# Optimization experiments

Measured on AMD Instinct MI355X. Metric: run time of the kernel, lower is better.

The kernel has to match this reference:

```python
import jax, jax.numpy as jnp
import numpy as np
from jax import lax

B, H, W, C, NH = 16, 56, 56, 192, 6
L = H * W
DH = C // NH            # 32
HID = 4 * C             # 768
ETA = 1.0 / DH          # TTT inner-loop learning rate
EPS = 1e-5

# ---- RoPE rotation tables (deterministic buffer, shape (H, W, C//2)) ----
_kmax = C // 4
_theta = 1.0 / (10000.0 ** (np.arange(_kmax) / _kmax))
_ii, _jj = np.meshgrid(np.arange(H), np.arange(W), indexing='ij')
_ang = np.concatenate([_ii[..., None] * _theta, _jj[..., None] * _theta], axis=-1)  # (H,W,C/2)
_COS = jnp.asarray(np.cos(_ang), dtype=jnp.float32)
_SIN = jnp.asarray(np.sin(_ang), dtype=jnp.float32)


def layernorm(x, g, b):
    mu = jnp.mean(x, axis=-1, keepdims=True)
    var = jnp.mean(jnp.square(x - mu), axis=-1, keepdims=True)
    return (x - mu) * lax.rsqrt(var + EPS) * g + b


def dwconv3x3(x_blc, w, b):
    # x: (B, L, Ch) -> depthwise 3x3 conv over (H, W) -> (B, L, Ch)
    Ch = x_blc.shape[-1]
    xi = x_blc.reshape(B, H, W, Ch).transpose(0, 3, 1, 2)  # NCHW
    y = lax.conv_general_dilated(xi, w, (1, 1), 'SAME', feature_group_count=Ch,
                                 dimension_numbers=('NCHW', 'OIHW', 'NCHW'))
    y = y + b[None, :, None, None]
    return y.transpose(0, 2, 3, 1).reshape(B, L, Ch)


def rope(x):
    # x: (B, L, C); rotate complex pairs with 2D axial angles
    xr = x.reshape(B, H, W, C // 2, 2)
    re, im = xr[..., 0], xr[..., 1]
    o_re = _COS * re - _SIN * im
    o_im = _SIN * re + _COS * im
    return jnp.stack([o_re, o_im], axis=-1).reshape(B, L, C)


def ttt_attn(xn, qkv_w, qkv_b, W0, proj_w, proj_b):
    qkv = xn @ qkv_w.T + qkv_b                      # (B, L, 3C)
    q, k, v = jnp.split(qkv, 3, axis=-1)
    q = rope(q) * (DH ** -0.5)
    k = rope(k)

    def to_heads(t):  # (B,L,C) -> (L, B*NH, DH)
        return t.reshape(B, L, NH, DH).transpose(1, 0, 2, 3).reshape(L, B * NH, DH)
    qs, ks, vs = to_heads(q), to_heads(k), to_heads(v)

    Wst0 = jnp.broadcast_to(W0[None], (B, NH, DH, DH)).reshape(B * NH, DH, DH)

    def step(Wst, qkv_t):
        qt, kt, vt = qkv_t
        pred = jnp.einsum('bij,bj->bi', Wst, kt)
        Wn = Wst - ETA * (pred - vt)[:, :, None] * kt[:, None, :]
        ot = jnp.einsum('bij,bj->bi', Wn, qt)
        return Wn, ot

    _, out = lax.scan(step, Wst0, (qs, ks, vs))     # out: (L, B*NH, DH)
    out = out.reshape(L, B, NH, DH).transpose(1, 0, 2, 3).reshape(B, L, C)
    return out @ proj_w.T + proj_b


def setup_inputs() -> dict:
    key = jax.random.key(0)
    ks = jax.random.split(key, 12)
    s = 0.02
    return {
        'x': jax.random.normal(ks[0], (B, L, C), jnp.float32),
        'cpe_w': jax.random.normal(ks[1], (C, 1, 3, 3), jnp.float32) * s,
        'cpe_b': jnp.zeros((C,), jnp.float32),
        'n1_g': jnp.ones((C,), jnp.float32),
        'n1_b': jnp.zeros((C,), jnp.float32),
        'qkv_w': jax.random.normal(ks[2], (3 * C, C), jnp.float32) * s,
        'qkv_b': jnp.zeros((3 * C,), jnp.float32),
        'W0': jax.random.normal(ks[3], (NH, DH, DH), jnp.float32) * s,
        'proj_w': jax.random.normal(ks[4], (C, C), jnp.float32) * s,
        'proj_b': jnp.zeros((C,), jnp.float32),
        'n2_g': jnp.ones((C,), jnp.float32),
        'n2_b': jnp.zeros((C,), jnp.float32),
        'fc1_w': jax.random.normal(ks[5], (HID, C), jnp.float32) * s,
        'fc1_b': jnp.zeros((HID,), jnp.float32),
        'dwc_w': jax.random.normal(ks[6], (HID, 1, 3, 3), jnp.float32) * s,
        'dwc_b': jnp.zeros((HID,), jnp.float32),
        'fc2_w': jax.random.normal(ks[7], (C, HID), jnp.float32) * s,
        'fc2_b': jnp.zeros((C,), jnp.float32),
    }


def reference(x, cpe_w, cpe_b, n1_g, n1_b, qkv_w, qkv_b, W0, proj_w, proj_b,
              n2_g, n2_b, fc1_w, fc1_b, dwc_w, dwc_b, fc2_w, fc2_b):
    # CPE: conditional positional encoding (depthwise conv residual)
    x = x + dwconv3x3(x, cpe_w, cpe_b)
    # TTT attention branch
    x = x + ttt_attn(layernorm(x, n1_g, n1_b), qkv_w, qkv_b, W0, proj_w, proj_b)
    # MLP branch with depthwise conv
    h1 = jax.nn.gelu(layernorm(x, n2_g, n2_b) @ fc1_w.T + fc1_b, approximate=False)
    h1 = jax.nn.gelu(h1 + dwconv3x3(h1, dwc_w, dwc_b), approximate=False)
    x = x + (h1 @ fc2_w.T + fc2_b)
    return x
```

## Files before the change

### kernel.cpp

```cpp
#include <hip/hip_runtime.h>
#include <hip/hip_bf16.h>

#define Bc 16
#define Hc 56
#define Wcc 56
#define Cc 192
#define NHc 6
#define Lc 3136
#define DHc 32
#define HIDc 768
#define NHEAD 96
#define Sc 32
#define NCHUNK 98
#define NPAIR (NHEAD*NCHUNK)
#define ROWS (Bc*Lc)
#define GR2 (ROWS/2)
#define ETAc (1.0f/32.0f)

typedef unsigned short u16;
typedef unsigned int u32;
typedef __attribute__((ext_vector_type(8))) short bf16x8;
typedef __attribute__((ext_vector_type(4))) float f32x4;
typedef __attribute__((ext_vector_type(16))) float f32x16;

__device__ __forceinline__ float b2f(u16 v){ u32 u = ((u32)v)<<16; float f; __builtin_memcpy(&f,&u,4); return f; }
__device__ __forceinline__ u16 f2b(float f){ u32 u; __builtin_memcpy(&u,&f,4); u32 r = u + 0x7FFFu + ((u>>16)&1u); return (u16)(r>>16); }
__device__ __forceinline__ f32x16 zero16(){ f32x16 z = {0,0,0,0,0,0,0,0,0,0,0,0,0,0,0,0}; return z; }

__device__ __forceinline__ void make_bfrags(const f32x16& t, int hi, bf16x8& b1, bf16x8& b2){
  u32 P[8], S[8];
  #pragma unroll
  for (int q=0;q<4;q++){
    #pragma unroll
    for (int j=0;j<2;j++){
      u32 r; float lo = t[4*q+2*j], hv = t[4*q+2*j+1];
      asm("v_cvt_pk_bf16_f32 %0, %1, %2" : "=v"(r) : "v"(lo), "v"(hv));
      P[2*q+j] = r;
    }
  }
  #pragma unroll
  for (int i=0;i<8;i++) S[i] = (u32)__shfl_xor((int)P[i], 32);
  union { u32 u[4]; bf16x8 v; } f1, f2;
  if (hi==0){ f1.u[0]=P[0]; f1.u[1]=P[1]; f1.u[2]=S[0]; f1.u[3]=S[1];
              f2.u[0]=P[4]; f2.u[1]=P[5]; f2.u[2]=S[4]; f2.u[3]=S[5]; }
  else      { f1.u[0]=S[2]; f1.u[1]=S[3]; f1.u[2]=P[2]; f1.u[3]=P[3];
              f2.u[0]=S[6]; f2.u[1]=S[7]; f2.u[2]=P[6]; f2.u[3]=P[7]; }
  b1 = f1.v; b2 = f2.v;
}

__global__ __launch_bounds__(256) void cast_bf16_kernel(const float* __restrict__ src, u16* __restrict__ dst, int n){
  int i = blockIdx.x*256 + threadIdx.x;
  if (i < n) dst[i] = f2b(src[i]);
}

__global__ __launch_bounds__(256) void dwt_kernel(const float* __restrict__ w, float* __restrict__ wt, int CH){
  int i = blockIdx.x*256 + threadIdx.x;
  if (i < CH*9){ int ch = i/9, t = i - ch*9; wt[t*CH + ch] = w[i]; }
}

__global__ __launch_bounds__(256) void rope_tab_kernel(float* __restrict__ ct, float* __restrict__ st){
  int i = blockIdx.x*256 + threadIdx.x;
  int l = i/96, p = i - l*96;
  int h = l/Wcc, w = l - h*Wcc;
  int kk = (p<48)? p : p-48;
  float th = powf(10000.f, -(float)kk/48.f);
  float ang = (float)((p<48)? h : w) * th;
  ct[i] = cosf(ang);
  st[i] = sinf(ang);
}

__global__ __launch_bounds__(256) void cpe_kernel(const float* __restrict__ x, const float* __restrict__ cwt9,
                                                  const float* __restrict__ bs, u16* __restrict__ x1){
  int gid = blockIdx.x*256 + threadIdx.x;
  int cg = gid % 24; int row = gid / 24; int ch0 = cg*8;
  int l = row % Lc; int h = l/Wcc, w = l - h*Wcc;
  const float* xp = x + (size_t)row*Cc + ch0;
  float acc[8];
  { f32x4 b0 = *(const f32x4*)(bs+ch0), b1v = *(const f32x4*)(bs+ch0+4);
    acc[0]=b0[0];acc[1]=b0[1];acc[2]=b0[2];acc[3]=b0[3];
    acc[4]=b1v[0];acc[5]=b1v[1];acc[6]=b1v[2];acc[7]=b1v[3]; }
  #pragma unroll
  for (int kh=0;kh<3;kh++){
    int hh = h+kh-1; if (hh<0 || hh>=Hc) continue;
    #pragma unroll
    for (int kw=0;kw<3;kw++){
      int ww = w+kw-1; if (ww<0 || ww>=Wcc) continue;
      const float* ip = xp + ((kh-1)*Wcc + (kw-1))*Cc;
      f32x4 i0 = *(const f32x4*)ip, i1 = *(const f32x4*)(ip+4);
      const float* wp = cwt9 + (kh*3+kw)*Cc + ch0;
      f32x4 w0 = *(const f32x4*)wp, w1 = *(const f32x4*)(wp+4);
      acc[0] += i0[0]*w0[0]; acc[1] += i0[1]*w0[1]; acc[2] += i0[2]*w0[2]; acc[3] += i0[3]*w0[3];
      acc[4] += i1[0]*w1[0]; acc[5] += i1[1]*w1[1]; acc[6] += i1[2]*w1[2]; acc[7] += i1[3]*w1[3];
    }
  }
  f32x4 c0 = *(const f32x4*)xp, c1 = *(const f32x4*)(xp+4);
  union { bf16x8 v; u16 s[8]; } ov;
  ov.s[0]=f2b(c0[0]+acc[0]); ov.s[1]=f2b(c0[1]+acc[1]); ov.s[2]=f2b(c0[2]+acc[2]); ov.s[3]=f2b(c0[3]+acc[3]);
  ov.s[4]=f2b(c1[0]+acc[4]); ov.s[5]=f2b(c1[1]+acc[5]); ov.s[6]=f2b(c1[2]+acc[6]); ov.s[7]=f2b(c1[3]+acc[7]);
  *(bf16x8*)(x1 + (size_t)row*Cc + ch0) = ov.v;
}

template<int INF32>
__global__ __launch_bounds__(256) void ln_kernel(const u16* __restrict__ xb, const float* __restrict__ xf,
                                                 const float* __restrict__ g, const float* __restrict__ b,
                                                 u16* __restrict__ out){
  int row = blockIdx.x*4 + (threadIdx.x>>6);
  int lane = threadIdx.x & 63;
  float v0, v1, v2;
  if (INF32){
    const float* xr = xf + (size_t)row*Cc;
    v0 = xr[lane]; v1 = xr[lane+64]; v2 = xr[lane+128];
  } else {
    const u16* xr = xb + (size_t)row*Cc;
    v0 = b2f(xr[lane]); v1 = b2f(xr[lane+64]); v2 = b2f(xr[lane+128]);
  }
  float s = v0+v1+v2;
  float q = v0*v0 + v1*v1 + v2*v2;
  #pragma unroll
  for (int off=32; off; off>>=1){ s += __shfl_xor(s, off); q += __shfl_xor(q, off); }
  float mu = s*(1.f/Cc);
  float var = q*(1.f/Cc) - mu*mu;
  float rs = rsqrtf(var + 1e-5f);
  u16* orow = out + (size_t)row*Cc;
  orow[lane]     = f2b((v0-mu)*rs*g[lane]     + b[lane]);
  orow[lane+64]  = f2b((v1-mu)*rs*g[lane+64]  + b[lane+64]);
  orow[lane+128] = f2b((v2-mu)*rs*g[lane+128] + b[lane+128]);
}

template<int MODE, int KT>
__global__ __launch_bounds__(256) void gemm_kernel(
    const u16* __restrict__ A, const u16* __restrict__ Wt,
    const float* __restrict__ bias,
    float* __restrict__ outf, u16* __restrict__ outb,
    u16* __restrict__ vdst, const u16* __restrict__ residb, const float* __restrict__ residf)
{
  constexpr int NCH = KT/192;
  __shared__ __align__(16) char smem[64*200*2];
  u16* As = (u16*)smem;
  float* Os32 = (float*)smem;
  u16* Osu = (u16*)smem;
  int tid = threadIdx.x;
  int wid = tid>>6, lane = tid&63;
  int wr = wid>>1, wc = wid&1;
  int m0 = blockIdx.x*64;
  int nblk = blockIdx.y*192;
  int n0 = nblk + wc*96;
  int ar = lane&15, kg = lane>>4;
  f32x4 acc[2][6];
  #pragma unroll
  for (int f=0;f<2;f++)
    #pragma unroll
    for (int c=0;c<6;c++){ f32x4 z = {0.f,0.f,0.f,0.f}; acc[f][c] = z; }
  bf16x8 bcur[6], bnxt[6];
  #pragma unroll
  for (int c=0;c<6;c++) bcur[c] = *(const bf16x8*)(Wt + (size_t)(n0 + c*16 + ar)*KT + kg*8);
  #pragma unroll
  for (int ch=0; ch<NCH; ch++){
    if (ch>0) __syncthreads();
    #pragma unroll
    for (int j=0;j<6;j++){
      int g = j*256 + tid;
      int grow = g/24, gcol = (g - grow*24)*8;
      bf16x8 v = *(const bf16x8*)(A + (size_t)(m0+grow)*KT + ch*192 + gcol);
      *(bf16x8*)(As + grow*200 + gcol) = v;
    }
    __syncthreads();
    #pragma unroll
    for (int kc=0;kc<6;kc++){
      int s = ch*6 + kc;
      if (s+1 < NCH*6){
        int koff = ((s+1)/6)*192 + ((s+1)%6)*32 + kg*8;
        #pragma unroll
        for (int c=0;c<6;c++) bnxt[c] = *(const bf16x8*)(Wt + (size_t)(n0 + c*16 + ar)*KT + koff);
      }
      bf16x8 af[2];
      #pragma unroll
      for (int f=0;f<2;f++)
        af[f] = *(const bf16x8*)(As + (wr*32 + f*16 + ar)*200 + kc*32 + kg*8);
      #pragma unroll
      for (int f=0;f<2;f++)
        #pragma unroll
        for (int c=0;c<6;c++)
          acc[f][c] = __builtin_amdgcn_mfma_f32_16x16x32_bf16(af[f], bcur[c], acc[f][c], 0,0,0);
      #pragma unroll
      for (int c=0;c<6;c++) bcur[c] = bnxt[c];
    }
  }
  __syncthreads();
  if (MODE==0 || MODE==2){
    #pragma unroll
    for (int f=0;f<2;f++){
      #pragma unroll
      for (int c=0;c<6;c++){
        float bv = bias[n0 + c*16 + ar];
        #pragma unroll
        for (int j=0;j<4;j++){
          float v = acc[f][c][j] + bv;
          if (MODE==2) v = 0.5f*v*(1.f + erff(v*0.70710678118654752f));
          Osu[(wr*32 + f*16 + kg*4 + j)*200 + wc*96 + c*16 + ar] = f2b(v);
        }
      }
    }
    __syncthreads();
    #pragma unroll
    for (int j=0;j<6;j++){
      int g = j*256 + tid;
      int grow = g/24, gcol = (g - grow*24)*8;
      bf16x8 v = *(const bf16x8*)(Osu + grow*200 + gcol);
      int row = m0 + grow, col = nblk + gcol;
      if (MODE==2){
        *(bf16x8*)(outb + (size_t)row*HIDc + col) = v;
      } else if (col < 384){
        *(bf16x8*)(outb + (size_t)row*384 + col) = v;
      } else {
        int bb = row/Lc; int l = row - bb*Lc;
        int nh = gcol>>5, d = gcol&31;
        *(bf16x8*)(vdst + (((size_t)(bb*NHc+nh))*Lc + l)*DHc + d) = v;
      }
    }
  } else {
    #pragma unroll
    for (int half=0; half<2; half++){
      if (wc==half){
        #pragma unroll
        for (int f=0;f<2;f++){
          #pragma unroll
          for (int c=0;c<6;c++){
            float bv = bias[n0 + c*16 + ar];
            #pragma unroll
            for (int j=0;j<4;j++)
              Os32[(wr*32 + f*16 + kg*4 + j)*100 + c*16 + ar] = acc[f][c][j] + bv;
          }
        }
      }
      __syncthreads();
      #pragma unroll
      for (int j=0;j<6;j++){
        int g = j*256 + tid;
        int grow = g/24, qcol = (g - grow*24)*4;
        f32x4 v = *(const f32x4*)(Os32 + grow*100 + qcol);
        int row = m0 + grow, colg = half*96 + qcol;
        if (MODE==1){
          const u16* rp = residb + (size_t)row*Cc + colg;
          v[0] += b2f(rp[0]); v[1] += b2f(rp[1]); v[2] += b2f(rp[2]); v[3] += b2f(rp[3]);
        } else {
          f32x4 rv = *(const f32x4*)(residf + (size_t)row*Cc + colg);
          v[0] += rv[0]; v[1] += rv[1]; v[2] += rv[2]; v[3] += rv[3];
        }
        *(f32x4*)(outf + (size_t)row*Cc + colg) = v;
      }
      if (half==0) __syncthreads();
    }
  }
}

__global__ __launch_bounds__(256) void rope_kernel(const u16* __restrict__ qk, const float* __restrict__ ct,
                                                   const float* __restrict__ st, u16* __restrict__ q_s, u16* __restrict__ k_s){
  int gid = blockIdx.x*256 + threadIdx.x;
  int sub = gid % 24; int row = gid / 24;
  int bb = row / Lc; int l = row - bb*Lc;
  bool isq = sub < 12; int pg = isq ? sub : sub-12;
  int p0 = pg*8;
  int cbase = (isq ? 0 : 192) + 2*p0;
  const u16* qr = qk + (size_t)row*384 + cbase;
  bf16x8 in0 = *(const bf16x8*)qr;
  bf16x8 in1 = *(const bf16x8*)(qr + 8);
  const float* cp = ct + l*96 + p0;
  const float* sp = st + l*96 + p0;
  f32x4 c0 = *(const f32x4*)cp, c1 = *(const f32x4*)(cp+4);
  f32x4 s0 = *(const f32x4*)sp, s1 = *(const f32x4*)(sp+4);
  float cs[8] = {c0[0],c0[1],c0[2],c0[3],c1[0],c1[1],c1[2],c1[3]};
  float sn[8] = {s0[0],s0[1],s0[2],s0[3],s1[0],s1[1],s1[2],s1[3]};
  float sc = isq ? 0.1767766952966369f : 1.0f;
  union { bf16x8 v; u16 s[8]; } o0, o1;
  #pragma unroll
  for (int j=0;j<4;j++){
    float re = b2f((u16)in0[2*j]), im = b2f((u16)in0[2*j+1]);
    o0.s[2*j]   = f2b((cs[j]*re - sn[j]*im)*sc);
    o0.s[2*j+1] = f2b((sn[j]*re + cs[j]*im)*sc);
  }
  #pragma unroll
  for (int j=0;j<4;j++){
    float re = b2f((u16)in1[2*j]), im = b2f((u16)in1[2*j+1]);
    o1.s[2*j]   = f2b((cs[4+j]*re - sn[4+j]*im)*sc);
    o1.s[2*j+1] = f2b((sn[4+j]*re + cs[4+j]*im)*sc);
  }
  int nh = pg>>1, d0 = (pg&1)*16;
  u16* dst = (isq ? q_s : k_s) + (((size_t)(bb*NHc+nh))*Lc + l)*DHc + d0;
  *(bf16x8*)dst = o0.v;
  *(bf16x8*)(dst+8) = o1.v;
}

__global__ __launch_bounds__(64) void ttta_kernel(const u16* __restrict__ k_s, const u16* __restrict__ v_s,
                                                  u16* __restrict__ u_s, u16* __restrict__ rn_s,
                                                  u16* __restrict__ af_s, u16* __restrict__ bc_s){
  __shared__ float Gl[1024];
  __shared__ u16 LK[32*40];
  __shared__ float LU[32*33];
  __shared__ float LR[32*33];
  int pair = blockIdx.x;
  int head = pair / NCHUNK;
  int l0 = (pair - head*NCHUNK) * Sc;
  int lane = threadIdx.x; int rr = lane&31; int hi = lane>>5; int ks = hi*8;
  const u16* kb = k_s + ((size_t)head*Lc + l0)*DHc;
  bf16x8 a0 = *(const bf16x8*)(kb + rr*32 + ks);
  bf16x8 a1 = *(const bf16x8*)(kb + rr*32 + 16 + ks);
  *(bf16x8*)(LK + rr*40 + ks) = a0;
  *(bf16x8*)(LK + rr*40 + 16 + ks) = a1;
  f32x16 g = zero16();
  g = __builtin_amdgcn_mfma_f32_32x32x16_bf16(a0, a0, g, 0,0,0);
  g = __builtin_amdgcn_mfma_f32_32x32x16_bf16(a1, a1, g, 0,0,0);
  #pragma unroll
  for (int reg=0;reg<16;reg++){
    int i = (reg&3) + 8*(reg>>2) + 4*hi;
    Gl[i*32 + rr] = ETAc * g[reg];
  }
  __syncthreads();
  float X[32];
  if (lane < 32){
    #pragma unroll
    for (int i=0;i<32;i++) X[i] = ETAc * b2f(v_s[((size_t)head*Lc + l0 + i)*DHc + lane]);
  } else {
    int m = lane-32;
    #pragma unroll
    for (int i=0;i<32;i++) X[i] = ETAc * b2f(kb[i*32 + m]);
  }
  #pragma unroll
  for (int i=1;i<32;i++){
    float a = X[i];
    #pragma unroll
    for (int j=0;j<i;j++) a -= Gl[i*32+j]*X[j];
    X[i] = a;
  }
  if (lane < 32){
    u16* dst = u_s + (size_t)pair*1024 + lane;
    #pragma unroll
    for (int i=0;i<32;i++) dst[i*32] = f2b(X[i]);
    #pragma unroll
    for (int i=0;i<32;i++) LU[lane*33 + i] = X[i];
  } else {
    u16* dst = rn_s + (size_t)pair*1024 + (lane&31);
    #pragma unroll
    for (int i=0;i<32;i++) dst[i*32] = f2b(-X[i]);
    #pragma unroll
    for (int i=0;i<32;i++) LR[(lane&31)*33 + i] = X[i];
  }
  __syncthreads();
  union { bf16x8 v; u16 s[8]; } kc1, kc2, uc1, uc2, rc1, rc2;
  #pragma unroll
  for (int s=0;s<8;s++){
    kc1.s[s] = LK[(ks+s)*40 + rr];
    kc2.s[s] = LK[(16+ks+s)*40 + rr];
    uc1.s[s] = f2b(LU[rr*33 + ks+s]);
    uc2.s[s] = f2b(LU[rr*33 + 16+ks+s]);
    rc1.s[s] = f2b(LR[rr*33 + ks+s]);
    rc2.s[s] = f2b(LR[rr*33 + 16+ks+s]);
  }
  f32x16 bacc = zero16();
  bacc = __builtin_amdgcn_mfma_f32_32x32x16_bf16(kc1.v, uc1.v, bacc, 0,0,0);
  bacc = __builtin_amdgcn_mfma_f32_32x32x16_bf16(kc2.v, uc2.v, bacc, 0,0,0);
  union { bf16x8 v; u16 s[8]; } bo1, bo2;
  #pragma unroll
  for (int r=0;r<8;r++){ bo1.s[r] = f2b(bacc[r]); bo2.s[r] = f2b(bacc[8+r]); }
  *(bf16x8*)(bc_s + (size_t)pair*1024 + lane*16) = bo1.v;
  *(bf16x8*)(bc_s + (size_t)pair*1024 + lane*16 + 8) = bo2.v;
  f32x16 aacc = zero16();
  aacc = __builtin_amdgcn_mfma_f32_32x32x16_bf16(rc1.v, kc1.v, aacc, 0,0,0);
  aacc = __builtin_amdgcn_mfma_f32_32x32x16_bf16(rc2.v, kc2.v, aacc, 0,0,0);
  f32x16 an;
  #pragma unroll
  for (int r=0;r<16;r++) an[r] = -aacc[r];
  bf16x8 f1, f2;
  make_bfrags(an, hi, f1, f2);
  *(bf16x8*)(af_s + (size_t)pair*1024 + lane*16) = f1;
  *(bf16x8*)(af_s + (size_t)pair*1024 + lane*16 + 8) = f2;
}

__global__ __launch_bounds__(64) void tttb_kernel(const u16* __restrict__ af_s, const u16* __restrict__ bc_s,
                                                  const float* __restrict__ W0, u16* __restrict__ w_snap){
  int head = blockIdx.x; int nh = head % NHc;
  int lane = threadIdx.x; int rr = lane&31; int hi = lane>>5;
  f32x16 T;
  const float* w0r = W0 + nh*1024 + rr*32 + 4*hi;
  #pragma unroll
  for (int q=0;q<4;q++){
    f32x4 v = *(const f32x4*)(w0r + 8*q);
    T[4*q+0]=v[0]; T[4*q+1]=v[1]; T[4*q+2]=v[2]; T[4*q+3]=v[3];
  }
  size_t hb = (size_t)head*NCHUNK;
  const bf16x8* afp = (const bf16x8*)(af_s + hb*1024);
  const bf16x8* bcp = (const bf16x8*)(bc_s + hb*1024);
  bf16x8 A1 = afp[lane*2], A2 = afp[lane*2+1];
  bf16x8 Bv1 = bcp[lane*2], Bv2 = bcp[lane*2+1];
  bf16x8 b1, b2;
  make_bfrags(T, hi, b1, b2);
  for (int c=0;c<NCHUNK;c++){
    bf16x8 nA1=A1, nA2=A2, nB1=Bv1, nB2=Bv2;
    if (c+1 < NCHUNK){
      int base = (c+1)*128 + lane*2;
      nA1 = afp[base]; nA2 = afp[base+1];
      nB1 = bcp[base]; nB2 = bcp[base+1];
    }
    u16* wrow = w_snap + (hb + c)*1024 + rr*32;
    *(bf16x8*)(wrow + hi*8) = b1;
    *(bf16x8*)(wrow + 16 + hi*8) = b2;
    f32x16 acc;
    #pragma unroll
    for (int r=0;r<8;r++){ acc[r] = T[r] + b2f((u16)Bv1[r]); acc[8+r] = T[8+r] + b2f((u16)Bv2[r]); }
    acc = __builtin_amdgcn_mfma_f32_32x32x16_bf16(A1, b1, acc, 0,0,0);
    acc = __builtin_amdgcn_mfma_f32_32x32x16_bf16(A2, b2, acc, 0,0,0);
    T = acc;
    make_bfrags(T, hi, b1, b2);
    A1=nA1; A2=nA2; Bv1=nB1; Bv2=nB2;
  }
}

__global__ __launch_bounds__(64) void tttc_kernel(const u16* __restrict__ q_s, const u16* __restrict__ k_s,
                                                  const u16* __restrict__ w_snap, const u16* __restrict__ u_s,
                                                  const u16* __restrict__ rn_s, u16* __restrict__ o_bf){
  __shared__ __align__(16) u16 Pl[32*40];
  int pair = blockIdx.x;
  int head = pair / NCHUNK;
  int ch = pair - head*NCHUNK;
  int l0 = ch*Sc;
  int lane = threadIdx.x; int rr = lane&31; int hi = lane>>5; int ks = hi*8;
  const u16* qb = q_s + ((size_t)head*Lc + l0)*DHc;
  const u16* kb = k_s + ((size_t)head*Lc + l0)*DHc;
  bf16x8 q0 = *(const bf16x8*)(qb + rr*32 + ks);
  bf16x8 q1 = *(const bf16x8*)(qb + rr*32 + 16 + ks);
  bf16x8 k0 = *(const bf16x8*)(kb + rr*32 + ks);
  bf16x8 k1 = *(const bf16x8*)(kb + rr*32 + 16 + ks);
  f32x16 p = zero16();
  p = __builtin_amdgcn_mfma_f32_32x32x16_bf16(q0, k0, p, 0,0,0);
  p = __builtin_amdgcn_mfma_f32_32x32x16_bf16(q1, k1, p, 0,0,0);
  #pragma unroll
  for (int reg=0;reg<16;reg++){
    int i = (reg&3)+8*(reg>>2)+4*hi;
    Pl[i*40+rr] = (rr<=i) ? f2b(p[reg]) : (u16)0;
  }
  const u16* wsb = w_snap + (size_t)pair*1024;
  bf16x8 tb0 = *(const bf16x8*)(wsb + rr*32 + ks);
  bf16x8 tb1 = *(const bf16x8*)(wsb + rr*32 + 16 + ks);
  const u16* ub = u_s + (size_t)pair*1024;
  f32x16 wr;
  #pragma unroll
  for (int r=0;r<16;r++){
    int i = (r&3)+8*(r>>2)+4*hi;
    wr[r] = b2f(ub[i*32 + rr]);
  }
  const u16* rb = rn_s + (size_t)pair*1024;
  bf16x8 rn0 = *(const bf16x8*)(rb + rr*32 + ks);
  bf16x8 rn1 = *(const bf16x8*)(rb + rr*32 + 16 + ks);
  wr = __builtin_amdgcn_mfma_f32_32x32x16_bf16(rn0, tb0, wr, 0,0,0);
  wr = __builtin_amdgcn_mfma_f32_32x32x16_bf16(rn1, tb1, wr, 0,0,0);
  bf16x8 wb0, wb1;
  make_bfrags(wr, hi, wb0, wb1);
  __syncthreads();
  f32x16 o = zero16();
  o = __builtin_amdgcn_mfma_f32_32x32x16_bf16(q0, tb0, o, 0,0,0);
  o = __builtin_amdgcn_mfma_f32_32x32x16_bf16(q1, tb1, o, 0,0,0);
  bf16x8 pa0 = *(const bf16x8*)(Pl + rr*40 + ks);
  bf16x8 pa1 = *(const bf16x8*)(Pl + rr*40 + 16 + ks);
  o = __builtin_amdgcn_mfma_f32_32x32x16_bf16(pa0, wb0, o, 0,0,0);
  o = __builtin_amdgcn_mfma_f32_32x32x16_bf16(pa1, wb1, o, 0,0,0);
  int bb = head/NHc, nh = head - bb*NHc;
  #pragma unroll
  for (int reg=0;reg<16;reg++){
    int i = (reg&3)+8*(reg>>2)+4*hi;
    o_bf[((size_t)(bb*Lc + l0 + i))*Cc + nh*32 + rr] = f2b(o[reg]);
  }
}

__global__ __launch_bounds__(256) void dwc_kernel(const u16* __restrict__ h1, const float* __restrict__ wt9,
                                                  const float* __restrict__ bs, u16* __restrict__ h2, int row0){
  int gid = blockIdx.x*256 + threadIdx.x;
  int cg = gid % 96; int lrow = gid / 96; int ch0 = cg*8;
  int row = row0 + lrow;
  int l = row % Lc; int h = l/Wcc, w = l - h*Wcc;
  const u16* hp = h1 + (size_t)lrow*HIDc + ch0;
  float acc[8];
  { f32x4 b0 = *(const f32x4*)(bs+ch0), b1v = *(const f32x4*)(bs+ch0+4);
    acc[0]=b0[0];acc[1]=b0[1];acc[2]=b0[2];acc[3]=b0[3];
    acc[4]=b1v[0];acc[5]=b1v[1];acc[6]=b1v[2];acc[7]=b1v[3]; }
  #pragma unroll
  for (int kh=0;kh<3;kh++){
    int hh = h+kh-1; if (hh<0 || hh>=Hc) continue;
    #pragma unroll
    for (int kw=0;kw<3;kw++){
      int ww = w+kw-1; if (ww<0 || ww>=Wcc) continue;
      bf16x8 iv = *(const bf16x8*)(hp + ((kh-1)*Wcc + (kw-1))*HIDc);
      const float* wp = wt9 + (kh*3+kw)*HIDc + ch0;
      f32x4 w0 = *(const f32x4*)wp, w1 = *(const f32x4*)(wp+4);
      acc[0] += b2f((u16)iv[0])*w0[0]; acc[1] += b2f((u16)iv[1])*w0[1];
      acc[2] += b2f((u16)iv[2])*w0[2]; acc[3] += b2f((u16)iv[3])*w0[3];
      acc[4] += b2f((u16)iv[4])*w1[0]; acc[5] += b2f((u16)iv[5])*w1[1];
      acc[6] += b2f((u16)iv[6])*w1[2]; acc[7] += b2f((u16)iv[7])*w1[3];
    }
  }
  bf16x8 cv = *(const bf16x8*)hp;
  union { bf16x8 v; u16 s[8]; } ov;
  #pragma unroll
  for (int j=0;j<8;j++){
    float v = b2f((u16)cv[j]) + acc[j];
    ov.s[j] = f2b(0.5f*v*(1.f + erff(v*0.70710678118654752f)));
  }
  *(bf16x8*)(h2 + (size_t)lrow*HIDc + ch0) = ov.v;
}

extern "C" void kernel_launch(void* const* d_in, const int* in_sizes, int n_in,
                              void* d_out, int out_size, void* d_ws, size_t ws_size,
                              hipStream_t stream){
  const float* x     = (const float*)d_in[0];
  const float* cpe_w = (const float*)d_in[1];
  const float* cpe_b = (const float*)d_in[2];
  const float* n1_g  = (const float*)d_in[3];
  const float* n1_b  = (const float*)d_in[4];
  const float* qkv_w = (const float*)d_in[5];
  const float* qkv_b = (const float*)d_in[6];
  const float* W0    = (const float*)d_in[7];
  const float* proj_w= (const float*)d_in[8];
  const float* proj_b= (const float*)d_in[9];
  const float* n2_g  = (const float*)d_in[10];
  const float* n2_b  = (const float*)d_in[11];
  const float* fc1_w = (const float*)d_in[12];
  const float* fc1_b = (const float*)d_in[13];
  const float* dwc_w = (const float*)d_in[14];
  const float* dwc_b = (const float*)d_in[15];
  const float* fc2_w = (const float*)d_in[16];
  const float* fc2_b = (const float*)d_in[17];

  char* ws = (char*)d_ws;
  size_t off = 0;
  auto alloc = [&](size_t bytes)->char*{
    char* p = ws + off;
    off += (bytes + 255) & ~(size_t)255;
    return p;
  };
  u16* wbqkv = (u16*)alloc((size_t)576*192*2);
  u16* wbproj= (u16*)alloc((size_t)192*192*2);
  u16* wbfc1 = (u16*)alloc((size_t)768*192*2);
  u16* wbfc2 = (u16*)alloc((size_t)192*768*2);
  float* dwt9 = (float*)alloc((size_t)9*HIDc*4);
  float* cwt9 = (float*)alloc((size_t)9*Cc*4);
  float* ctab = (float*)alloc((size_t)Lc*96*4);
  float* stab = (float*)alloc((size_t)Lc*96*4);
  u16* regA = (u16*)alloc((size_t)ROWS*Cc*2);
  u16* regB = (u16*)alloc((size_t)ROWS*Cc*2);
  u16* regD = (u16*)alloc((size_t)NHEAD*Lc*DHc*2);
  u16* regE = (u16*)alloc((size_t)NHEAD*Lc*DHc*2);
  u16* rn_s = (u16*)alloc((size_t)NPAIR*1024*2);
  u16* af_s = (u16*)alloc((size_t)NPAIR*1024*2);
  u16* wsn  = (u16*)alloc((size_t)NPAIR*1024*2);
  u16* qk = (u16*)d_out;
  u16* us = (u16*)d_out;
  u16* bc = us + (size_t)NPAIR*1024;
  float* x2 = (float*)d_out;

  u16* x1 = regA;
  u16* xn = regB;
  u16* qs = regB;
  u16* xn2 = regB;
  u16* vs = regD;
  u16* obf = regD;
  u16* ksb = regE;
  u16* h1 = regD;
  u16* h2 = rn_s;

  cast_bf16_kernel<<<(576*192+255)/256,256,0,stream>>>(qkv_w, wbqkv, 576*192);
  cast_bf16_kernel<<<(192*192+255)/256,256,0,stream>>>(proj_w, wbproj, 192*192);
  cast_bf16_kernel<<<(768*192+255)/256,256,0,stream>>>(fc1_w, wbfc1, 768*192);
  cast_bf16_kernel<<<(192*768+255)/256,256,0,stream>>>(fc2_w, wbfc2, 192*768);
  dwt_kernel<<<(768*9+255)/256,256,0,stream>>>(dwc_w, dwt9, HIDc);
  dwt_kernel<<<(192*9+255)/256,256,0,stream>>>(cpe_w, cwt9, Cc);
  rope_tab_kernel<<<(Lc*96)/256,256,0,stream>>>(ctab, stab);

  cpe_kernel<<<(ROWS*24)/256,256,0,stream>>>(x, cwt9, cpe_b, x1);
  ln_kernel<0><<<ROWS/4,256,0,stream>>>(x1, nullptr, n1_g, n1_b, xn);
  { dim3 g(ROWS/64, 3); gemm_kernel<0,192><<<g,256,0,stream>>>(xn, wbqkv, qkv_b, nullptr, qk, vs, nullptr, nullptr); }
  rope_kernel<<<(ROWS*24)/256,256,0,stream>>>(qk, ctab, stab, qs, ksb);
  ttta_kernel<<<NPAIR,64,0,stream>>>(ksb, vs, us, rn_s, af_s, bc);
  tttb_kernel<<<NHEAD,64,0,stream>>>(af_s, bc, W0, wsn);
  tttc_kernel<<<NPAIR,64,0,stream>>>(qs, ksb, wsn, us, rn_s, obf);
  { dim3 g(ROWS/64, 1); gemm_kernel<1,192><<<g,256,0,stream>>>(obf, wbproj, proj_b, x2, nullptr, nullptr, x1, nullptr); }
  ln_kernel<1><<<ROWS/4,256,0,stream>>>(nullptr, x2, n2_g, n2_b, xn2);
  for (int g4=0; g4<2; g4++){
    const u16* a_in = xn2 + (size_t)g4*GR2*Cc;
    float* xo = x2 + (size_t)g4*GR2*Cc;
    { dim3 g(GR2/64, 4); gemm_kernel<2,192><<<g,256,0,stream>>>(a_in, wbfc1, fc1_b, nullptr, h1, nullptr, nullptr, nullptr); }
    dwc_kernel<<<(GR2*96)/256,256,0,stream>>>(h1, dwt9, dwc_b, h2, g4*GR2);
    { dim3 g(GR2/64, 1); gemm_kernel<3,768><<<g,256,0,stream>>>(h2, wbfc2, fc2_b, xo, nullptr, nullptr, nullptr, xo); }
  }
}
```

Measured before the change: 526.2 us.

## Fuse CPE with LayerNorm, RoPE into QKV epilogue, and merge weight prep kernels

Merges the six weight cast/transpose launches into one prep kernel. Fuses the CPE depthwise conv with the first LayerNorm, and moves RoPE and q-scaling into the QKV GEMM epilogue so q/k go straight to head-major layout, removing the intermediate qk buffer and the separate rope kernel. The proj GEMM now writes the residual sum as bf16 instead of fp32, and that bf16 buffer feeds both LN2 and the fc2 residual. This cuts launches and intermediate traffic, at the cost of rounding the post-attention residual stream to bf16 and a workspace layout with more aliasing.

```diff
diff --git a/kernel.cpp b/kernel.cpp
--- a/kernel.cpp
+++ b/kernel.cpp
@@ -48,14 +48,19 @@
   b1 = f1.v; b2 = f2.v;
 }
 
-__global__ __launch_bounds__(256) void cast_bf16_kernel(const float* __restrict__ src, u16* __restrict__ dst, int n){
+__global__ __launch_bounds__(256) void prep_kernel(
+    const float* __restrict__ qkvw, const float* __restrict__ projw,
+    const float* __restrict__ fc1w, const float* __restrict__ fc2w,
+    const float* __restrict__ dwcw, const float* __restrict__ cpew,
+    u16* __restrict__ wbqkv, u16* __restrict__ wbproj, u16* __restrict__ wbfc1,
+    u16* __restrict__ wbfc2, float* __restrict__ dwt9, float* __restrict__ cwt9){
   int i = blockIdx.x*256 + threadIdx.x;
-  if (i < n) dst[i] = f2b(src[i]);
-}
-
-__global__ __launch_bounds__(256) void dwt_kernel(const float* __restrict__ w, float* __restrict__ wt, int CH){
-  int i = blockIdx.x*256 + threadIdx.x;
-  if (i < CH*9){ int ch = i/9, t = i - ch*9; wt[t*CH + ch] = w[i]; }
+  if (i < 110592) wbqkv[i] = f2b(qkvw[i]);
+  else if (i < 147456){ int j=i-110592; wbproj[j] = f2b(projw[j]); }
+  else if (i < 294912){ int j=i-147456; wbfc1[j] = f2b(fc1w[j]); }
+  else if (i < 442368){ int j=i-294912; wbfc2[j] = f2b(fc2w[j]); }
+  else if (i < 449280){ int j=i-442368; int ch=j/9, t=j-ch*9; dwt9[t*HIDc+ch] = dwcw[j]; }
+  else if (i < 451008){ int j=i-449280; int ch=j/9, t=j-ch*9; cwt9[t*Cc+ch] = cpew[j]; }
 }
 
 __global__ __launch_bounds__(256) void rope_tab_kernel(float* __restrict__ ct, float* __restrict__ st){
@@ -69,10 +74,14 @@
   st[i] = sinf(ang);
 }
 
-__global__ __launch_bounds__(256) void cpe_kernel(const float* __restrict__ x, const float* __restrict__ cwt9,
-                                                  const float* __restrict__ bs, u16* __restrict__ x1){
-  int gid = blockIdx.x*256 + threadIdx.x;
-  int cg = gid % 24; int row = gid / 24; int ch0 = cg*8;
+__global__ __launch_bounds__(192) void cpe_ln_kernel(const float* __restrict__ x, const float* __restrict__ cwt9,
+                                                     const float* __restrict__ bs, const float* __restrict__ g,
+                                                     const float* __restrict__ b,
+                                                     u16* __restrict__ x1, u16* __restrict__ xn){
+  __shared__ float ps[192], pq[192], smu[8], srs[8];
+  int tid = threadIdx.x;
+  int rl = tid/24, sub = tid - rl*24, ch0 = sub*8;
+  int row = blockIdx.x*8 + rl;
   int l = row % Lc; int h = l/Wcc, w = l - h*Wcc;
   const float* xp = x + (size_t)row*Cc + ch0;
   float acc[8];
@@ -93,46 +102,66 @@
       acc[4] += i1[0]*w1[0]; acc[5] += i1[1]*w1[1]; acc[6] += i1[2]*w1[2]; acc[7] += i1[3]*w1[3];
     }
   }
-  f32x4 c0 = *(const f32x4*)xp, c1 = *(const f32x4*)(xp+4);
-  union { bf16x8 v; u16 s[8]; } ov;
-  ov.s[0]=f2b(c0[0]+acc[0]); ov.s[1]=f2b(c0[1]+acc[1]); ov.s[2]=f2b(c0[2]+acc[2]); ov.s[3]=f2b(c0[3]+acc[3]);
-  ov.s[4]=f2b(c1[0]+acc[4]); ov.s[5]=f2b(c1[1]+acc[5]); ov.s[6]=f2b(c1[2]+acc[6]); ov.s[7]=f2b(c1[3]+acc[7]);
-  *(bf16x8*)(x1 + (size_t)row*Cc + ch0) = ov.v;
-}
-
-template<int INF32>
-__global__ __launch_bounds__(256) void ln_kernel(const u16* __restrict__ xb, const float* __restrict__ xf,
-                                                 const float* __restrict__ g, const float* __restrict__ b,
-                                                 u16* __restrict__ out){
+  float val[8];
+  { f32x4 c0 = *(const f32x4*)xp, c1 = *(const f32x4*)(xp+4);
+    val[0]=c0[0]+acc[0]; val[1]=c0[1]+acc[1]; val[2]=c0[2]+acc[2]; val[3]=c0[3]+acc[3];
+    val[4]=c1[0]+acc[4]; val[5]=c1[1]+acc[5]; val[6]=c1[2]+acc[6]; val[7]=c1[3]+acc[7]; }
+  float s8=0.f, q8=0.f;
+  #pragma unroll
+  for (int j=0;j<8;j++){ s8 += val[j]; q8 += val[j]*val[j]; }
+  ps[tid]=s8; pq[tid]=q8;
+  __syncthreads();
+  if (tid < 8){
+    float s=0.f, q=0.f;
+    #pragma unroll
+    for (int k=0;k<24;k++){ s += ps[tid*24+k]; q += pq[tid*24+k]; }
+    float mu = s*(1.f/Cc);
+    float var = q*(1.f/Cc) - mu*mu;
+    smu[tid] = mu; srs[tid] = rsqrtf(var + 1e-5f);
+  }
+  __syncthreads();
+  float mu = smu[rl], rstd = srs[rl];
+  union { bf16x8 v; u16 s[8]; } o1, o2;
+  f32x4 g0 = *(const f32x4*)(g+ch0), g1 = *(const f32x4*)(g+ch0+4);
+  f32x4 bb0 = *(const f32x4*)(b+ch0), bb1 = *(const f32x4*)(b+ch0+4);
+  float gg[8] = {g0[0],g0[1],g0[2],g0[3],g1[0],g1[1],g1[2],g1[3]};
+  float bbv[8] = {bb0[0],bb0[1],bb0[2],bb0[3],bb1[0],bb1[1],bb1[2],bb1[3]};
+  #pragma unroll
+  for (int j=0;j<8;j++){
+    o1.s[j] = f2b(val[j]);
+    o2.s[j] = f2b((val[j]-mu)*rstd*gg[j] + bbv[j]);
+  }
+  *(bf16x8*)(x1 + (size_t)row*Cc + ch0) = o1.v;
+  *(bf16x8*)(xn + (size_t)row*Cc + ch0) = o2.v;
+}
+
+__global__ __launch_bounds__(256) void ln_kernel(const u16* __restrict__ xb, const float* __restrict__ g,
+                                                 const float* __restrict__ b, u16* __restrict__ out){
   int row = blockIdx.x*4 + (threadIdx.x>>6);
   int lane = threadIdx.x & 63;
-  float v0, v1, v2;
-  if (INF32){
-    const float* xr = xf + (size_t)row*Cc;
-    v0 = xr[lane]; v1 = xr[lane+64]; v2 = xr[lane+128];
-  } else {
-    const u16* xr = xb + (size_t)row*Cc;
-    v0 = b2f(xr[lane]); v1 = b2f(xr[lane+64]); v2 = b2f(xr[lane+128]);
-  }
+  const u16* xr = xb + (size_t)row*Cc;
+  float v0 = b2f(xr[lane]), v1 = b2f(xr[lane+64]), v2 = b2f(xr[lane+128]);
   float s = v0+v1+v2;
   float q = v0*v0 + v1*v1 + v2*v2;
   #pragma unroll
   for (int off=32; off; off>>=1){ s += __shfl_xor(s, off); q += __shfl_xor(q, off); }
   float mu = s*(1.f/Cc);
   float var = q*(1.f/Cc) - mu*mu;
-  float rs = rsqrtf(var + 1e-5f);
+  float rstd = rsqrtf(var + 1e-5f);
   u16* orow = out + (size_t)row*Cc;
-  orow[lane]     = f2b((v0-mu)*rs*g[lane]     + b[lane]);
-  orow[lane+64]  = f2b((v1-mu)*rs*g[lane+64]  + b[lane+64]);
-  orow[lane+128] = f2b((v2-mu)*rs*g[lane+128] + b[lane+128]);
+  orow[lane]     = f2b((v0-mu)*rstd*g[lane]     + b[lane]);
+  orow[lane+64]  = f2b((v1-mu)*rstd*g[lane+64]  + b[lane+64]);
+  orow[lane+128] = f2b((v2-mu)*rstd*g[lane+128] + b[lane+128]);
 }
 
 template<int MODE, int KT>
 __global__ __launch_bounds__(256) void gemm_kernel(
     const u16* __restrict__ A, const u16* __restrict__ Wt,
     const float* __restrict__ bias,
-    float* __restrict__ outf, u16* __restrict__ outb,
-    u16* __restrict__ vdst, const u16* __restrict__ residb, const float* __restrict__ residf)
+    float* __restrict__ outf, u16* __restrict__ outb, u16* __restrict__ vdst,
+    const u16* __restrict__ residb,
+    const float* __restrict__ ct, const float* __restrict__ st,
+    u16* __restrict__ q_s, u16* __restrict__ k_s)
 {
   constexpr int NCH = KT/192;
   __shared__ __align__(16) char smem[64*200*2];
@@ -187,7 +216,7 @@
     }
   }
   __syncthreads();
-  if (MODE==0 || MODE==2){
+  if (MODE != 3){
     #pragma unroll
     for (int f=0;f<2;f++){
       #pragma unroll
@@ -207,15 +236,37 @@
       int g = j*256 + tid;
       int grow = g/24, gcol = (g - grow*24)*8;
       bf16x8 v = *(const bf16x8*)(Osu + grow*200 + gcol);
-      int row = m0 + grow, col = nblk + gcol;
+      int row = m0 + grow;
       if (MODE==2){
-        *(bf16x8*)(outb + (size_t)row*HIDc + col) = v;
-      } else if (col < 384){
-        *(bf16x8*)(outb + (size_t)row*384 + col) = v;
+        *(bf16x8*)(outb + (size_t)row*HIDc + nblk + gcol) = v;
+      } else if (MODE==1){
+        const u16* rp = residb + (size_t)row*Cc + gcol;
+        bf16x8 rv = *(const bf16x8*)rp;
+        union { bf16x8 v; u16 s[8]; } o;
+        #pragma unroll
+        for (int t=0;t<8;t++) o.s[t] = f2b(b2f((u16)v[t]) + b2f((u16)rv[t]));
+        *(bf16x8*)(outb + (size_t)row*Cc + gcol) = o.v;
       } else {
         int bb = row/Lc; int l = row - bb*Lc;
         int nh = gcol>>5, d = gcol&31;
-        *(bf16x8*)(vdst + (((size_t)(bb*NHc+nh))*Lc + l)*DHc + d) = v;
+        if (nblk < 384){
+          bool isq = (nblk == 0);
+          int p0 = gcol>>1;
+          f32x4 cv = *(const f32x4*)(ct + l*96 + p0);
+          f32x4 sv = *(const f32x4*)(st + l*96 + p0);
+          float sc = isq ? 0.1767766952966369f : 1.0f;
+          union { bf16x8 v; u16 s[8]; } o;
+          #pragma unroll
+          for (int t=0;t<4;t++){
+            float re = b2f((u16)v[2*t]), im = b2f((u16)v[2*t+1]);
+            o.s[2*t]   = f2b((cv[t]*re - sv[t]*im)*sc);
+            o.s[2*t+1] = f2b((sv[t]*re + cv[t]*im)*sc);
+          }
+          u16* dst = (isq ? q_s : k_s) + (((size_t)(bb*NHc+nh))*Lc + l)*DHc + d;
+          *(bf16x8*)dst = o.v;
+        } else {
+          *(bf16x8*)(vdst + (((size_t)(bb*NHc+nh))*Lc + l)*DHc + d) = v;
+        }
       }
     }
   } else {
@@ -240,55 +291,13 @@
         int grow = g/24, qcol = (g - grow*24)*4;
         f32x4 v = *(const f32x4*)(Os32 + grow*100 + qcol);
         int row = m0 + grow, colg = half*96 + qcol;
-        if (MODE==1){
-          const u16* rp = residb + (size_t)row*Cc + colg;
-          v[0] += b2f(rp[0]); v[1] += b2f(rp[1]); v[2] += b2f(rp[2]); v[3] += b2f(rp[3]);
-        } else {
-          f32x4 rv = *(const f32x4*)(residf + (size_t)row*Cc + colg);
-          v[0] += rv[0]; v[1] += rv[1]; v[2] += rv[2]; v[3] += rv[3];
-        }
+        const u16* rp = residb + (size_t)row*Cc + colg;
+        v[0] += b2f(rp[0]); v[1] += b2f(rp[1]); v[2] += b2f(rp[2]); v[3] += b2f(rp[3]);
         *(f32x4*)(outf + (size_t)row*Cc + colg) = v;
       }
       if (half==0) __syncthreads();
     }
   }
-}
-
-__global__ __launch_bounds__(256) void rope_kernel(const u16* __restrict__ qk, const float* __restrict__ ct,
-                                                   const float* __restrict__ st, u16* __restrict__ q_s, u16* __restrict__ k_s){
-  int gid = blockIdx.x*256 + threadIdx.x;
-  int sub = gid % 24; int row = gid / 24;
-  int bb = row / Lc; int l = row - bb*Lc;
-  bool isq = sub < 12; int pg = isq ? sub : sub-12;
-  int p0 = pg*8;
-  int cbase = (isq ? 0 : 192) + 2*p0;
-  const u16* qr = qk + (size_t)row*384 + cbase;
-  bf16x8 in0 = *(const bf16x8*)qr;
-  bf16x8 in1 = *(const bf16x8*)(qr + 8);
-  const float* cp = ct + l*96 + p0;
-  const float* sp = st + l*96 + p0;
-  f32x4 c0 = *(const f32x4*)cp, c1 = *(const f32x4*)(cp+4);
-  f32x4 s0 = *(const f32x4*)sp, s1 = *(const f32x4*)(sp+4);
-  float cs[8] = {c0[0],c0[1],c0[2],c0[3],c1[0],c1[1],c1[2],c1[3]};
-  float sn[8] = {s0[0],s0[1],s0[2],s0[3],s1[0],s1[1],s1[2],s1[3]};
-  float sc = isq ? 0.1767766952966369f : 1.0f;
-  union { bf16x8 v; u16 s[8]; } o0, o1;
-  #pragma unroll
-  for (int j=0;j<4;j++){
-    float re = b2f((u16)in0[2*j]), im = b2f((u16)in0[2*j+1]);
-    o0.s[2*j]   = f2b((cs[j]*re - sn[j]*im)*sc);
-    o0.s[2*j+1] = f2b((sn[j]*re + cs[j]*im)*sc);
-  }
-  #pragma unroll
-  for (int j=0;j<4;j++){
-    float re = b2f((u16)in1[2*j]), im = b2f((u16)in1[2*j+1]);
-    o1.s[2*j]   = f2b((cs[4+j]*re - sn[4+j]*im)*sc);
-    o1.s[2*j+1] = f2b((sn[4+j]*re + cs[4+j]*im)*sc);
-  }
-  int nh = pg>>1, d0 = (pg&1)*16;
-  u16* dst = (isq ? q_s : k_s) + (((size_t)(bb*NHc+nh))*Lc + l)*DHc + d0;
-  *(bf16x8*)dst = o0.v;
-  *(bf16x8*)(dst+8) = o1.v;
 }
 
 __global__ __launch_bounds__(64) void ttta_kernel(const u16* __restrict__ k_s, const u16* __restrict__ v_s,
@@ -546,48 +555,47 @@
   float* stab = (float*)alloc((size_t)Lc*96*4);
   u16* regA = (u16*)alloc((size_t)ROWS*Cc*2);
   u16* regB = (u16*)alloc((size_t)ROWS*Cc*2);
+  u16* regC = (u16*)alloc((size_t)NHEAD*Lc*DHc*2);
   u16* regD = (u16*)alloc((size_t)NHEAD*Lc*DHc*2);
   u16* regE = (u16*)alloc((size_t)NHEAD*Lc*DHc*2);
   u16* rn_s = (u16*)alloc((size_t)NPAIR*1024*2);
   u16* af_s = (u16*)alloc((size_t)NPAIR*1024*2);
-  u16* wsn  = (u16*)alloc((size_t)NPAIR*1024*2);
-  u16* qk = (u16*)d_out;
   u16* us = (u16*)d_out;
   u16* bc = us + (size_t)NPAIR*1024;
-  float* x2 = (float*)d_out;
 
   u16* x1 = regA;
+  u16* x2b = regA;
   u16* xn = regB;
-  u16* qs = regB;
+  u16* obf = regB;
   u16* xn2 = regB;
+  u16* qs = regC;
   u16* vs = regD;
-  u16* obf = regD;
+  u16* wsn = regD;
   u16* ksb = regE;
   u16* h1 = regD;
   u16* h2 = rn_s;
 
-  cast_bf16_kernel<<<(576*192+255)/256,256,0,stream>>>(qkv_w, wbqkv, 576*192);
-  cast_bf16_kernel<<<(192*192+255)/256,256,0,stream>>>(proj_w, wbproj, 192*192);
-  cast_bf16_kernel<<<(768*192+255)/256,256,0,stream>>>(fc1_w, wbfc1, 768*192);
-  cast_bf16_kernel<<<(192*768+255)/256,256,0,stream>>>(fc2_w, wbfc2, 192*768);
-  dwt_kernel<<<(768*9+255)/256,256,0,stream>>>(dwc_w, dwt9, HIDc);
-  dwt_kernel<<<(192*9+255)/256,256,0,stream>>>(cpe_w, cwt9, Cc);
+  prep_kernel<<<(451008+255)/256,256,0,stream>>>(qkv_w, proj_w, fc1_w, fc2_w, dwc_w, cpe_w,
+                                                 wbqkv, wbproj, wbfc1, wbfc2, dwt9, cwt9);
   rope_tab_kernel<<<(Lc*96)/256,256,0,stream>>>(ctab, stab);
 
-  cpe_kernel<<<(ROWS*24)/256,256,0,stream>>>(x, cwt9, cpe_b, x1);
-  ln_kernel<0><<<ROWS/4,256,0,stream>>>(x1, nullptr, n1_g, n1_b, xn);
-  { dim3 g(ROWS/64, 3); gemm_kernel<0,192><<<g,256,0,stream>>>(xn, wbqkv, qkv_b, nullptr, qk, vs, nullptr, nullptr); }
-  rope_kernel<<<(ROWS*24)/256,256,0,stream>>>(qk, ctab, stab, qs, ksb);
+  cpe_ln_kernel<<<ROWS/8,192,0,stream>>>(x, cwt9, cpe_b, n1_g, n1_b, x1, xn);
+  { dim3 g(ROWS/64, 3); gemm_kernel<0,192><<<g,256,0,stream>>>(xn, wbqkv, qkv_b,
+      nullptr, nullptr, vs, nullptr, ctab, stab, qs, ksb); }
   ttta_kernel<<<NPAIR,64,0,stream>>>(ksb, vs, us, rn_s, af_s, bc);
   tttb_kernel<<<NHEAD,64,0,stream>>>(af_s, bc, W0, wsn);
   tttc_kernel<<<NPAIR,64,0,stream>>>(qs, ksb, wsn, us, rn_s, obf);
-  { dim3 g(ROWS/64, 1); gemm_kernel<1,192><<<g,256,0,stream>>>(obf, wbproj, proj_b, x2, nullptr, nullptr, x1, nullptr); }
-  ln_kernel<1><<<ROWS/4,256,0,stream>>>(nullptr, x2, n2_g, n2_b, xn2);
+  { dim3 g(ROWS/64, 1); gemm_kernel<1,192><<<g,256,0,stream>>>(obf, wbproj, proj_b,
+      nullptr, x2b, nullptr, x1, nullptr, nullptr, nullptr, nullptr); }
+  ln_kernel<<<ROWS/4,256,0,stream>>>(x2b, n2_g, n2_b, xn2);
   for (int g4=0; g4<2; g4++){
     const u16* a_in = xn2 + (size_t)g4*GR2*Cc;
-    float* xo = x2 + (size_t)g4*GR2*Cc;
-    { dim3 g(GR2/64, 4); gemm_kernel<2,192><<<g,256,0,stream>>>(a_in, wbfc1, fc1_b, nullptr, h1, nullptr, nullptr, nullptr); }
+    float* xo = (float*)d_out + (size_t)g4*GR2*Cc;
+    const u16* res = x2b + (size_t)g4*GR2*Cc;
+    { dim3 g(GR2/64, 4); gemm_kernel<2,192><<<g,256,0,stream>>>(a_in, wbfc1, fc1_b,
+        nullptr, h1, nullptr, nullptr, nullptr, nullptr, nullptr, nullptr); }
     dwc_kernel<<<(GR2*96)/256,256,0,stream>>>(h1, dwt9, dwc_b, h2, g4*GR2);
-    { dim3 g(GR2/64, 1); gemm_kernel<3,768><<<g,256,0,stream>>>(h2, wbfc2, fc2_b, xo, nullptr, nullptr, nullptr, xo); }
-  }
-}
+    { dim3 g(GR2/64, 1); gemm_kernel<3,768><<<g,256,0,stream>>>(h2, wbfc2, fc2_b,
+        xo, nullptr, nullptr, res, nullptr, nullptr, nullptr, nullptr); }
+  }
+}
```

Result: faster. 503.3 us (-4.4%).
